# Optimization experiments

Measured on AMD Instinct MI355X. Metric: run time of the kernel, lower is better.

Reference implementation:

```python
import jax, jax.numpy as jnp
import numpy as np

N, NPER, B, E = 65536, 1024, 64, 1048576
IN_F, HID, K, NCLS = 128, 64, 16, 10


def setup_inputs() -> dict:
    key = jax.random.key(0)
    ks = jax.random.split(key, 12)
    x = jax.random.normal(ks[0], (N, IN_F), jnp.float32)
    # block-structured intra-graph edges: 64 graphs of 1024 contiguous nodes
    gid = jax.random.randint(ks[1], (E,), 0, B)
    src = gid * NPER + jax.random.randint(ks[2], (E,), 0, NPER)
    dst = gid * NPER + jax.random.randint(ks[3], (E,), 0, NPER)
    edge_index = jnp.stack([src, dst]).astype(jnp.int32)
    batch = (jnp.arange(N, dtype=jnp.int32) // NPER).astype(jnp.int32)
    def lin(k, fo, fi):
        kw, kb = jax.random.split(k)
        s = 1.0 / np.sqrt(fi)
        return (jax.random.uniform(kw, (fo, fi), jnp.float32, -s, s),
                jax.random.uniform(kb, (fo,), jnp.float32, -s, s))
    W1, b1 = lin(ks[4], HID, IN_F)
    W2, b2 = lin(ks[5], HID, HID)
    Wp, bp = lin(ks[6], K, HID)      # DMoN cluster-assignment MLP (single Linear)
    Wl, bl = lin(ks[7], NCLS, HID)   # final classifier
    return {"x": x, "edge_index": edge_index, "batch": batch,
            "W1": W1, "b1": b1, "W2": W2, "b2": b2,
            "Wp": Wp, "bp": bp, "Wl": Wl, "bl": bl}


def gcn_conv(x, src, dst, W, b):
    # GCNConv with add_self_loops=True, symmetric normalization
    n = x.shape[0]
    deg = jax.ops.segment_sum(jnp.ones(src.shape[0], x.dtype), dst,
                              num_segments=n) + 1.0  # +1 for self-loop
    dinv = jax.lax.rsqrt(deg)
    h = x @ W.T
    coef = (dinv[src] * dinv[dst])[:, None]
    agg = jax.ops.segment_sum(h[src] * coef, dst, num_segments=n)
    agg = agg + h * (dinv * dinv)[:, None]  # self-loop contribution
    return agg + b


def reference(x, edge_index, batch, W1, b1, W2, b2, Wp, bp, Wl, bl):
    src, dst = edge_index[0], edge_index[1]
    h = jax.nn.relu(gcn_conv(x, src, dst, W1, b1))
    h = jax.nn.relu(gcn_conv(h, src, dst, W2, b2))
    # to_dense_batch: graphs are equal-sized and contiguous -> reshape, mask all True
    Xb = h.reshape(B, NPER, HID)
    # DMoN cluster assignment (dropout=0.0, mask all ones)
    s = jax.nn.softmax(Xb @ Wp.T + bp, axis=-1)          # [B, NPER, K]
    Xp = jax.nn.selu(jnp.einsum('bnk,bnh->bkh', s, Xb))   # pooled clusters [B, K, HID]
    out = Xp.mean(axis=1)                                  # [B, HID]
    logits = out @ Wl.T + bl                               # [B, NCLS]
    return logits
```

## Files before the change

### kernel.cpp

```cpp
#include <hip/hip_runtime.h>
#include <cstddef>

#define N_NODES 65536
#define NPER    1024
#define NGRAPH  64
#define HID     64
#define IN_F    128
#define KCLUS   16
#define NCLS    10
#define ECAP    20480
#define HSTRIDE 12
#define ZROW    NPER
#define LIN_BLOCKS 512

template <int K>
__device__ __forceinline__ void gemm_tile(const float* __restrict__ X,
                                          const float* __restrict__ W,
                                          float* __restrict__ Y,
                                          float (*xs)[68], float (*ws)[68],
                                          int block, int t) {
    const size_t row0 = (size_t)block * 128;
    const int rbase = t >> 3;
    const int cbase = t & 7;
    float acc[4][8] = {};

    for (int kc = 0; kc < K; kc += 64) {
        __syncthreads();
        for (int i = t; i < 128 * 16; i += 256) {
            int row = i >> 4, k4 = (i & 15) << 2;
            *(float4*)&xs[row][k4] = *(const float4*)(X + (row0 + row) * K + kc + k4);
        }
        for (int i = t; i < 64 * 16; i += 256) {
            int col = i >> 4, k4 = (i & 15) << 2;
            *(float4*)&ws[col][k4] = *(const float4*)(W + col * K + kc + k4);
        }
        __syncthreads();

#pragma unroll 4
        for (int k4 = 0; k4 < 64; k4 += 4) {
            float4 xr[4], wr[8];
#pragma unroll
            for (int rr = 0; rr < 4; ++rr) xr[rr] = *(const float4*)&xs[rbase + 32 * rr][k4];
#pragma unroll
            for (int cc = 0; cc < 8; ++cc) wr[cc] = *(const float4*)&ws[cbase + 8 * cc][k4];
#pragma unroll
            for (int rr = 0; rr < 4; ++rr)
#pragma unroll
                for (int cc = 0; cc < 8; ++cc) {
                    acc[rr][cc] = fmaf(xr[rr].x, wr[cc].x, acc[rr][cc]);
                    acc[rr][cc] = fmaf(xr[rr].y, wr[cc].y, acc[rr][cc]);
                    acc[rr][cc] = fmaf(xr[rr].z, wr[cc].z, acc[rr][cc]);
                    acc[rr][cc] = fmaf(xr[rr].w, wr[cc].w, acc[rr][cc]);
                }
        }
    }

#pragma unroll
    for (int rr = 0; rr < 4; ++rr)
#pragma unroll
        for (int cc = 0; cc < 8; ++cc)
            Y[(row0 + rbase + 32 * rr) * HID + cbase + 8 * cc] = acc[rr][cc];
}

__global__ __launch_bounds__(256) void front_kernel(const float* __restrict__ X,
                                                    const float* __restrict__ W,
                                                    float* __restrict__ Y,
                                                    const int* __restrict__ src,
                                                    const int* __restrict__ dst,
                                                    int* __restrict__ ecnt,
                                                    int* __restrict__ gedges, int E) {
    __shared__ float xs[128][68];
    __shared__ float ws[64][68];
    const int t = threadIdx.x;

    if (blockIdx.x >= LIN_BLOCKS) {
        int* hist = (int*)&xs[0][0];
        int* base_l = hist + NGRAPH;
        const int e0 = (blockIdx.x - LIN_BLOCKS) * 1024;
        if (t < NGRAPH) hist[t] = 0;
        __syncthreads();

        int gg[4], rr[4], pk[4];
#pragma unroll
        for (int i = 0; i < 4; ++i) {
            int idx = e0 + i * 256 + t;
            if (idx < E) {
                int d = dst[idx], s = src[idx];
                int g = d >> 10;
                gg[i] = g;
                pk[i] = ((d & 1023) << 10) | (s & 1023);
                rr[i] = atomicAdd(&hist[g], 1);
            } else gg[i] = -1;
        }
        __syncthreads();
        if (t < NGRAPH) base_l[t] = atomicAdd(&ecnt[t], hist[t]);
        __syncthreads();
#pragma unroll
        for (int i = 0; i < 4; ++i) {
            if (gg[i] >= 0) {
                int pos = base_l[gg[i]] + rr[i];
                if (pos < ECAP) gedges[gg[i] * ECAP + pos] = pk[i];
            }
        }
        return;
    }

    gemm_tile<IN_F>(X, W, Y, xs, ws, blockIdx.x, t);
}

template <int K>
__global__ __launch_bounds__(256) void linear_kernel(const float* __restrict__ X,
                                                     const float* __restrict__ W,
                                                     float* __restrict__ Y) {
    __shared__ float xs[128][68];
    __shared__ float ws[64][68];
    gemm_tile<K>(X, W, Y, xs, ws, blockIdx.x, threadIdx.x);
}

__global__ __launch_bounds__(1024) void csr_kernel(const int* __restrict__ gedges,
                                                   const int* __restrict__ ecnt,
                                                   int* __restrict__ rp,
                                                   unsigned short* __restrict__ esorted,
                                                   float* __restrict__ dinv) {
    __shared__ int hist[NPER];
    __shared__ int wsum[16];
    const int g = blockIdx.x, t = threadIdx.x;
    const int lane = t & 63, wid = t >> 6;
    const int ec = ecnt[g];
    const int* ge = gedges + (size_t)g * ECAP;

    hist[t] = 0;
    __syncthreads();
    for (int i = t; i < ec; i += 1024) atomicAdd(&hist[ge[i] >> 10], 1);
    __syncthreads();

    const int h0 = hist[t];
    const int pd = (h0 + 3) & ~3;
    int v = pd;
#pragma unroll
    for (int off = 1; off < 64; off <<= 1) {
        int x = __shfl_up(v, off, 64);
        if (lane >= off) v += x;
    }
    if (lane == 63) wsum[wid] = v;
    __syncthreads();
    if (wid == 0) {
        int wv = (lane < 16) ? wsum[lane] : 0;
#pragma unroll
        for (int off = 1; off < 16; off <<= 1) {
            int x = __shfl_up(wv, off, 64);
            if (lane >= off) wv += x;
        }
        if (lane < 16) wsum[lane] = wv;
    }
    __syncthreads();
    const int incl = v + (wid > 0 ? wsum[wid - 1] : 0);
    const int excl = incl - pd;

    rp[g * (NPER + 1) + t] = excl;
    if (t == NPER - 1) rp[g * (NPER + 1) + NPER] = incl;
    dinv[g * NPER + t] = rsqrtf((float)h0 + 1.0f);

    hist[t] = excl;
    __syncthreads();

    unsigned short* es = esorted + (size_t)g * ECAP;
    for (int i = t; i < ec; i += 1024) {
        int pk = ge[i];
        int pos = atomicAdd(&hist[pk >> 10], 1);
        es[pos] = (unsigned short)(pk & 1023);
    }
    __syncthreads();
    for (int q = excl + h0; q < excl + pd; ++q) es[q] = (unsigned short)ZROW;
}

__global__ __launch_bounds__(512) void agg_kernel(const float* __restrict__ h,
                                                  const unsigned short* __restrict__ esorted,
                                                  const int* __restrict__ rp,
                                                  const float* __restrict__ dinv,
                                                  const float* __restrict__ bias,
                                                  float* __restrict__ outp) {
    __shared__ float Hs[(NPER + 1) * HSTRIDE];
    __shared__ float dl[NPER];
    const int g = blockIdx.x & 63;
    const int f0 = (blockIdx.x >> 6) * 8;
    const int t = threadIdx.x;
    const int base = g * NPER;

    for (int r = t; r < NPER; r += 512) {
        const float* hp = h + (size_t)(base + r) * HID + f0;
        float4 a = *(const float4*)hp;
        float4 b = *(const float4*)(hp + 4);
        float dv = dinv[base + r];
        dl[r] = dv;
        float* row = &Hs[r * HSTRIDE];
        *(float4*)row = make_float4(a.x * dv, a.y * dv, a.z * dv, a.w * dv);
        *(float4*)(row + 4) = make_float4(b.x * dv, b.y * dv, b.z * dv, b.w * dv);
    }
    if (t < HSTRIDE) Hs[ZROW * HSTRIDE + t] = 0.f;
    float bb[8];
#pragma unroll
    for (int j = 0; j < 8; ++j) bb[j] = bias[f0 + j];
    const unsigned short* es = esorted + (size_t)g * ECAP;
    const int* rpg = rp + g * (NPER + 1);
    __syncthreads();

    for (int ld = t; ld < NPER; ld += 512) {
        int p = rpg[ld];
        const int pe = rpg[ld + 1];
        const float* srow = &Hs[ld * HSTRIDE];
        float4 acc0 = *(const float4*)srow;
        float4 acc1 = *(const float4*)(srow + 4);
        float4 bcc0 = make_float4(0.f, 0.f, 0.f, 0.f);
        float4 bcc1 = make_float4(0.f, 0.f, 0.f, 0.f);

        for (; p < pe; p += 4) {
            uint2 w4 = *(const uint2*)(es + p);
            const float* r0 = &Hs[(int)(w4.x & 0xFFFFu) * HSTRIDE];
            const float* r1 = &Hs[(int)(w4.x >> 16) * HSTRIDE];
            const float* r2 = &Hs[(int)(w4.y & 0xFFFFu) * HSTRIDE];
            const float* r3 = &Hs[(int)(w4.y >> 16) * HSTRIDE];
            float4 a0 = *(const float4*)r0, a1 = *(const float4*)(r0 + 4);
            float4 b0 = *(const float4*)r1, b1 = *(const float4*)(r1 + 4);
            float4 c0v = *(const float4*)r2, c1v = *(const float4*)(r2 + 4);
            float4 d0 = *(const float4*)r3, d1 = *(const float4*)(r3 + 4);
            acc0.x += a0.x; acc0.y += a0.y; acc0.z += a0.z; acc0.w += a0.w;
            acc1.x += a1.x; acc1.y += a1.y; acc1.z += a1.z; acc1.w += a1.w;
            bcc0.x += b0.x; bcc0.y += b0.y; bcc0.z += b0.z; bcc0.w += b0.w;
            bcc1.x += b1.x; bcc1.y += b1.y; bcc1.z += b1.z; bcc1.w += b1.w;
            acc0.x += c0v.x; acc0.y += c0v.y; acc0.z += c0v.z; acc0.w += c0v.w;
            acc1.x += c1v.x; acc1.y += c1v.y; acc1.z += c1v.z; acc1.w += c1v.w;
            bcc0.x += d0.x; bcc0.y += d0.y; bcc0.z += d0.z; bcc0.w += d0.w;
            bcc1.x += d1.x; bcc1.y += d1.y; bcc1.z += d1.z; bcc1.w += d1.w;
        }
        acc0.x += bcc0.x; acc0.y += bcc0.y; acc0.z += bcc0.z; acc0.w += bcc0.w;
        acc1.x += bcc1.x; acc1.y += bcc1.y; acc1.z += bcc1.z; acc1.w += bcc1.w;

        const float dv = dl[ld];
        float4 o0, o1;
        o0.x = fmaxf(fmaf(acc0.x, dv, bb[0]), 0.f);
        o0.y = fmaxf(fmaf(acc0.y, dv, bb[1]), 0.f);
        o0.z = fmaxf(fmaf(acc0.z, dv, bb[2]), 0.f);
        o0.w = fmaxf(fmaf(acc0.w, dv, bb[3]), 0.f);
        o1.x = fmaxf(fmaf(acc1.x, dv, bb[4]), 0.f);
        o1.y = fmaxf(fmaf(acc1.y, dv, bb[5]), 0.f);
        o1.z = fmaxf(fmaf(acc1.z, dv, bb[6]), 0.f);
        o1.w = fmaxf(fmaf(acc1.w, dv, bb[7]), 0.f);
        float* op = outp + (size_t)(base + ld) * HID + f0;
        *(float4*)op = o0;
        *(float4*)(op + 4) = o1;
    }
}

__global__ __launch_bounds__(256) void pool1_kernel(const float* __restrict__ h,
                                                    const float* __restrict__ Wp,
                                                    const float* __restrict__ bp,
                                                    float* __restrict__ xpart) {
    __shared__ float xs[128][HID + 1];
    __shared__ float ss[128][KCLUS + 1];
    __shared__ float wp[KCLUS][HID];
    __shared__ float bps[KCLUS];
    const int g = blockIdx.x >> 3;
    const int c = blockIdx.x & 7;
    const int t = threadIdx.x;
    const float* hb = h + ((size_t)g * NPER + c * 128) * HID;

    for (int i = t; i < 128 * HID / 4; i += 256) {
        float4 v = ((const float4*)hb)[i];
        int row = i >> 4, col = (i & 15) * 4;
        xs[row][col] = v.x; xs[row][col + 1] = v.y; xs[row][col + 2] = v.z; xs[row][col + 3] = v.w;
    }
    for (int i = t; i < KCLUS * HID; i += 256) wp[i >> 6][i & 63] = Wp[i];
    if (t < KCLUS) bps[t] = bp[t];
    __syncthreads();

    if (t < 128) {
        float lg[KCLUS];
        float mx = -1e30f;
#pragma unroll
        for (int k = 0; k < KCLUS; ++k) {
            float a = bps[k];
#pragma unroll 8
            for (int hh = 0; hh < HID; ++hh) a = fmaf(xs[t][hh], wp[k][hh], a);
            lg[k] = a;
            mx = fmaxf(mx, a);
        }
        float sum = 0.f;
#pragma unroll
        for (int k = 0; k < KCLUS; ++k) {
            lg[k] = __expf(lg[k] - mx);
            sum += lg[k];
        }
        float inv = 1.0f / sum;
#pragma unroll
        for (int k = 0; k < KCLUS; ++k) ss[t][k] = lg[k] * inv;
    }
    __syncthreads();

    const int hcol = t & 63;
    const int k0 = (t >> 6) * 4;
    float a0 = 0.f, a1 = 0.f, a2 = 0.f, a3 = 0.f;
#pragma unroll 8
    for (int n = 0; n < 128; ++n) {
        float xv = xs[n][hcol];
        a0 = fmaf(ss[n][k0 + 0], xv, a0);
        a1 = fmaf(ss[n][k0 + 1], xv, a1);
        a2 = fmaf(ss[n][k0 + 2], xv, a2);
        a3 = fmaf(ss[n][k0 + 3], xv, a3);
    }
    float* xp = xpart + (((size_t)(g * 8 + c)) * KCLUS + k0) * HID + hcol;
    xp[0] = a0; xp[HID] = a1; xp[2 * HID] = a2; xp[3 * HID] = a3;
}

__global__ __launch_bounds__(256) void pool2_kernel(const float* __restrict__ xpart,
                                                    const float* __restrict__ Wl,
                                                    const float* __restrict__ bl,
                                                    float* __restrict__ out) {
    __shared__ float xp[KCLUS][HID + 1];
    __shared__ float outm[HID];
    const int g = blockIdx.x;
    const int t = threadIdx.x;
    const int hcol = t & 63;
    const int k0 = (t >> 6) * 4;
    const float* base = xpart + (size_t)g * 8 * KCLUS * HID;

    float a[4] = {};
#pragma unroll
    for (int c = 0; c < 8; ++c)
#pragma unroll
        for (int j = 0; j < 4; ++j)
            a[j] += base[(c * KCLUS + k0 + j) * HID + hcol];

    const float sc = 1.0507009873554805f, al = 1.6732632423543772f;
#pragma unroll
    for (int j = 0; j < 4; ++j) {
        float v = a[j];
        xp[k0 + j][hcol] = v > 0.f ? sc * v : sc * al * (__expf(v) - 1.f);
    }
    __syncthreads();

    if (t < HID) {
        float m = 0.f;
#pragma unroll
        for (int k = 0; k < KCLUS; ++k) m += xp[k][t];
        outm[t] = m * (1.0f / KCLUS);
    }
    __syncthreads();

    if (t < NCLS) {
        float acc = bl[t];
#pragma unroll 8
        for (int hh = 0; hh < HID; ++hh) acc = fmaf(outm[hh], Wl[t * HID + hh], acc);
        out[g * NCLS + t] = acc;
    }
}

extern "C" void kernel_launch(void* const* d_in, const int* in_sizes, int n_in,
                              void* d_out, int out_size, void* d_ws, size_t ws_size,
                              hipStream_t stream) {
    const float* x  = (const float*)d_in[0];
    const int* eidx = (const int*)d_in[1];
    const float* W1 = (const float*)d_in[3];
    const float* b1 = (const float*)d_in[4];
    const float* W2 = (const float*)d_in[5];
    const float* b2 = (const float*)d_in[6];
    const float* Wp = (const float*)d_in[7];
    const float* bp = (const float*)d_in[8];
    const float* Wl = (const float*)d_in[9];
    const float* bl = (const float*)d_in[10];
    float* out = (float*)d_out;

    const int E = in_sizes[1] / 2;
    const int* src = eidx;
    const int* dst = eidx + E;

    char* w = (char*)d_ws;
    int*            ecnt    = (int*)w;            w += 256;
    int*            gedges  = (int*)w;            w += (size_t)NGRAPH * ECAP * 4;
    unsigned short* esorted = (unsigned short*)w; w += (size_t)NGRAPH * ECAP * 2;
    int*            rp      = (int*)w;            w += (size_t)NGRAPH * (NPER + 1) * 4;
    float*          dinv    = (float*)w;          w += (size_t)N_NODES * 4;
    float*          A       = (float*)w;          w += (size_t)N_NODES * HID * 4;
    float*          Bf      = (float*)w;          w += (size_t)N_NODES * HID * 4;
    float*          xpart   = (float*)w;          w += (size_t)NGRAPH * 8 * KCLUS * HID * 4;

    hipMemsetAsync(ecnt, 0, 256, stream);

    const int nbucket = (E + 1023) / 1024;
    front_kernel<<<LIN_BLOCKS + nbucket, 256, 0, stream>>>(x, W1, A, src, dst, ecnt, gedges, E);
    csr_kernel<<<NGRAPH, 1024, 0, stream>>>(gedges, ecnt, rp, esorted, dinv);

    agg_kernel<<<NGRAPH * 8, 512, 0, stream>>>(A, esorted, rp, dinv, b1, Bf);

    linear_kernel<HID><<<N_NODES / 128, 256, 0, stream>>>(Bf, W2, A);
    agg_kernel<<<NGRAPH * 8, 512, 0, stream>>>(A, esorted, rp, dinv, b2, Bf);

    pool1_kernel<<<NGRAPH * 8, 256, 0, stream>>>(Bf, Wp, bp, xpart);
    pool2_kernel<<<NGRAPH, 256, 0, stream>>>(xpart, Wl, bl, out);
}
```

Measured before the change: 217.5 us.

## Fuse whole GCN pipeline into one cooperative persistent kernel with grid syncs

Replaces the seven separate kernel launches plus memset with a single cooperative mega-kernel of 512 blocks of 512 threads. Phases are separated by grid.sync(). The kernel zeroes counters in-kernel and changes CSR building to a deg/cursor atomic scatter. The intent is to remove per-launch gaps and host overhead between stages. The cost is that every phase is now tied to a fixed 512-block grid with larger blocks, and there are nine grid-wide barriers. It falls back to the old path if cooperative launch is not possible.

After: 213.9 us. Within noise of the previous version (-1.7%).

```diff
diff --git a/kernel.cpp b/kernel.cpp
--- a/kernel.cpp
+++ b/kernel.cpp
@@ -1,5 +1,8 @@
 #include <hip/hip_runtime.h>
+#include <hip/hip_cooperative_groups.h>
 #include <cstddef>
+
+namespace cg = cooperative_groups;
 
 #define N_NODES 65536
 #define NPER    1024
@@ -12,6 +15,8 @@
 #define HSTRIDE 12
 #define ZROW    NPER
 #define LIN_BLOCKS 512
+#define MGRID   512
+#define MBLK    512
 
 template <int K>
 __device__ __forceinline__ void gemm_tile(const float* __restrict__ X,
@@ -355,6 +360,346 @@
     }
 }
 
+
+struct SmGemm  { float xs[128][68]; float ws[64][68]; };
+struct SmAgg   { float Hs[(NPER + 1) * HSTRIDE]; float dl[NPER]; };
+struct SmBkt   { int hist[NGRAPH]; int base[NGRAPH]; };
+struct SmScan  { int wsum[8]; };
+struct SmPool1 { float xs[128][HID + 1]; float ss[128][KCLUS + 1];
+                 float wp[KCLUS][HID]; float bps[KCLUS]; };
+struct SmPool2 { float xp[KCLUS][HID + 1]; float outm[HID]; };
+union  SmAll   { SmGemm g; SmAgg a; SmBkt b; SmScan s; SmPool1 p1; SmPool2 p2; };
+
+struct MegaArgs {
+    const float* x; const int* src; const int* dst;
+    const float* W1; const float* b1; const float* W2; const float* b2;
+    const float* Wp; const float* bp; const float* Wl; const float* bl;
+    int* ecnt; int* gedges; int* deg; int* cursor; int* rp;
+    unsigned short* esorted; float* dinv; float* A; float* Bf; float* xpart;
+    float* out; int E;
+};
+
+template <int K>
+__device__ __forceinline__ void gemm512(const float* __restrict__ X,
+                                        const float* __restrict__ W,
+                                        float* __restrict__ Y,
+                                        float (*xs)[68], float (*ws)[68],
+                                        int block, int t) {
+    const size_t row0 = (size_t)block * 128;
+    const int rbase = t >> 3;
+    const int cbase = t & 7;
+    float acc[2][8] = {};
+
+    for (int kc = 0; kc < K; kc += 64) {
+        __syncthreads();
+        for (int i = t; i < 128 * 16; i += MBLK) {
+            int row = i >> 4, k4 = (i & 15) << 2;
+            *(float4*)&xs[row][k4] = *(const float4*)(X + (row0 + row) * K + kc + k4);
+        }
+        for (int i = t; i < 64 * 16; i += MBLK) {
+            int col = i >> 4, k4 = (i & 15) << 2;
+            *(float4*)&ws[col][k4] = *(const float4*)(W + col * K + kc + k4);
+        }
+        __syncthreads();
+
+#pragma unroll 4
+        for (int k4 = 0; k4 < 64; k4 += 4) {
+            float4 xr[2], wr[8];
+#pragma unroll
+            for (int rr = 0; rr < 2; ++rr) xr[rr] = *(const float4*)&xs[rbase + 64 * rr][k4];
+#pragma unroll
+            for (int cc = 0; cc < 8; ++cc) wr[cc] = *(const float4*)&ws[cbase + 8 * cc][k4];
+#pragma unroll
+            for (int rr = 0; rr < 2; ++rr)
+#pragma unroll
+                for (int cc = 0; cc < 8; ++cc) {
+                    acc[rr][cc] = fmaf(xr[rr].x, wr[cc].x, acc[rr][cc]);
+                    acc[rr][cc] = fmaf(xr[rr].y, wr[cc].y, acc[rr][cc]);
+                    acc[rr][cc] = fmaf(xr[rr].z, wr[cc].z, acc[rr][cc]);
+                    acc[rr][cc] = fmaf(xr[rr].w, wr[cc].w, acc[rr][cc]);
+                }
+        }
+    }
+
+#pragma unroll
+    for (int rr = 0; rr < 2; ++rr)
+#pragma unroll
+        for (int cc = 0; cc < 8; ++cc)
+            Y[(row0 + rbase + 64 * rr) * HID + cbase + 8 * cc] = acc[rr][cc];
+}
+
+__device__ __forceinline__ void agg_phase(const float* __restrict__ h,
+                                          const unsigned short* __restrict__ esorted,
+                                          const int* __restrict__ rp,
+                                          const float* __restrict__ dinv,
+                                          const float* __restrict__ bias,
+                                          float* __restrict__ outp,
+                                          SmAgg& s, int bid, int t) {
+    const int g = bid & 63;
+    const int f0 = (bid >> 6) * 8;
+    const int base = g * NPER;
+
+    for (int r = t; r < NPER; r += MBLK) {
+        const float* hp = h + (size_t)(base + r) * HID + f0;
+        float4 a = *(const float4*)hp;
+        float4 b = *(const float4*)(hp + 4);
+        float dv = dinv[base + r];
+        s.dl[r] = dv;
+        float* row = &s.Hs[r * HSTRIDE];
+        *(float4*)row = make_float4(a.x * dv, a.y * dv, a.z * dv, a.w * dv);
+        *(float4*)(row + 4) = make_float4(b.x * dv, b.y * dv, b.z * dv, b.w * dv);
+    }
+    if (t < HSTRIDE) s.Hs[ZROW * HSTRIDE + t] = 0.f;
+    float bb[8];
+#pragma unroll
+    for (int j = 0; j < 8; ++j) bb[j] = bias[f0 + j];
+    const unsigned short* es = esorted + (size_t)g * ECAP;
+    const int* rpg = rp + g * (NPER + 1);
+    __syncthreads();
+
+    for (int ld = t; ld < NPER; ld += MBLK) {
+        int p = rpg[ld];
+        const int pe = rpg[ld + 1];
+        const float* srow = &s.Hs[ld * HSTRIDE];
+        float4 acc0 = *(const float4*)srow;
+        float4 acc1 = *(const float4*)(srow + 4);
+        float4 bcc0 = make_float4(0.f, 0.f, 0.f, 0.f);
+        float4 bcc1 = make_float4(0.f, 0.f, 0.f, 0.f);
+
+        for (; p < pe; p += 4) {
+            uint2 w4 = *(const uint2*)(es + p);
+            const float* r0 = &s.Hs[(int)(w4.x & 0xFFFFu) * HSTRIDE];
+            const float* r1 = &s.Hs[(int)(w4.x >> 16) * HSTRIDE];
+            const float* r2 = &s.Hs[(int)(w4.y & 0xFFFFu) * HSTRIDE];
+            const float* r3 = &s.Hs[(int)(w4.y >> 16) * HSTRIDE];
+            float4 a0 = *(const float4*)r0, a1 = *(const float4*)(r0 + 4);
+            float4 b0 = *(const float4*)r1, b1 = *(const float4*)(r1 + 4);
+            float4 c0v = *(const float4*)r2, c1v = *(const float4*)(r2 + 4);
+            float4 d0 = *(const float4*)r3, d1 = *(const float4*)(r3 + 4);
+            acc0.x += a0.x; acc0.y += a0.y; acc0.z += a0.z; acc0.w += a0.w;
+            acc1.x += a1.x; acc1.y += a1.y; acc1.z += a1.z; acc1.w += a1.w;
+            bcc0.x += b0.x; bcc0.y += b0.y; bcc0.z += b0.z; bcc0.w += b0.w;
+            bcc1.x += b1.x; bcc1.y += b1.y; bcc1.z += b1.z; bcc1.w += b1.w;
+            acc0.x += c0v.x; acc0.y += c0v.y; acc0.z += c0v.z; acc0.w += c0v.w;
+            acc1.x += c1v.x; acc1.y += c1v.y; acc1.z += c1v.z; acc1.w += c1v.w;
+            bcc0.x += d0.x; bcc0.y += d0.y; bcc0.z += d0.z; bcc0.w += d0.w;
+            bcc1.x += d1.x; bcc1.y += d1.y; bcc1.z += d1.z; bcc1.w += d1.w;
+        }
+        acc0.x += bcc0.x; acc0.y += bcc0.y; acc0.z += bcc0.z; acc0.w += bcc0.w;
+        acc1.x += bcc1.x; acc1.y += bcc1.y; acc1.z += bcc1.z; acc1.w += bcc1.w;
+
+        const float dv = s.dl[ld];
+        float4 o0, o1;
+        o0.x = fmaxf(fmaf(acc0.x, dv, bb[0]), 0.f);
+        o0.y = fmaxf(fmaf(acc0.y, dv, bb[1]), 0.f);
+        o0.z = fmaxf(fmaf(acc0.z, dv, bb[2]), 0.f);
+        o0.w = fmaxf(fmaf(acc0.w, dv, bb[3]), 0.f);
+        o1.x = fmaxf(fmaf(acc1.x, dv, bb[4]), 0.f);
+        o1.y = fmaxf(fmaf(acc1.y, dv, bb[5]), 0.f);
+        o1.z = fmaxf(fmaf(acc1.z, dv, bb[6]), 0.f);
+        o1.w = fmaxf(fmaf(acc1.w, dv, bb[7]), 0.f);
+        float* op = outp + (size_t)(base + ld) * HID + f0;
+        *(float4*)op = o0;
+        *(float4*)(op + 4) = o1;
+    }
+}
+
+__global__ __launch_bounds__(MBLK, 4) void mega_kernel(MegaArgs a) {
+    cg::grid_group grid = cg::this_grid();
+    __shared__ SmAll sm;
+    const int bid = blockIdx.x;
+    const int t = threadIdx.x;
+
+    {
+        int gid = bid * MBLK + t;
+        if (gid < NGRAPH) a.ecnt[gid] = 0;
+        if (gid < N_NODES) a.deg[gid] = 0;
+    }
+    grid.sync();
+
+    {
+        int* hist = sm.b.hist;
+        int* basel = sm.b.base;
+        if (t < NGRAPH) hist[t] = 0;
+        __syncthreads();
+        int gg[4], rr2[4], pk[4];
+        const int e0 = bid * 2048;
+#pragma unroll
+        for (int i = 0; i < 4; ++i) {
+            int idx = e0 + i * MBLK + t;
+            if (idx < a.E) {
+                int d = a.dst[idx], s = a.src[idx];
+                int g = d >> 10;
+                gg[i] = g;
+                pk[i] = ((d & 1023) << 10) | (s & 1023);
+                rr2[i] = atomicAdd(&hist[g], 1);
+                atomicAdd(&a.deg[d], 1);
+            } else gg[i] = -1;
+        }
+        __syncthreads();
+        if (t < NGRAPH) basel[t] = atomicAdd(&a.ecnt[t], hist[t]);
+        __syncthreads();
+#pragma unroll
+        for (int i = 0; i < 4; ++i)
+            if (gg[i] >= 0) {
+                int pos = basel[gg[i]] + rr2[i];
+                if (pos < ECAP) a.gedges[gg[i] * ECAP + pos] = pk[i];
+            }
+    }
+    gemm512<IN_F>(a.x, a.W1, a.A, sm.g.xs, sm.g.ws, bid, t);
+    grid.sync();
+
+    if (bid < NGRAPH) {
+        const int g = bid;
+        int2 dd = *(const int2*)(a.deg + g * NPER + 2 * t);
+        const int d0 = dd.x, d1 = dd.y;
+        const int pd0 = (d0 + 3) & ~3, pd1 = (d1 + 3) & ~3;
+        const int v = pd0 + pd1;
+        const int lane = t & 63, w = t >> 6;
+        int vs = v;
+#pragma unroll
+        for (int off = 1; off < 64; off <<= 1) {
+            int xv = __shfl_up(vs, off, 64);
+            if (lane >= off) vs += xv;
+        }
+        if (lane == 63) sm.s.wsum[w] = vs;
+        __syncthreads();
+        if (t < 8) {
+            int wv = sm.s.wsum[t];
+#pragma unroll
+            for (int off = 1; off < 8; off <<= 1) {
+                int xv = __shfl_up(wv, off, 8);
+                if (t >= off) wv += xv;
+            }
+            sm.s.wsum[t] = wv;
+        }
+        __syncthreads();
+        const int incl = vs + (w > 0 ? sm.s.wsum[w - 1] : 0);
+        const int excl = incl - v;
+        const int e1 = excl + pd0;
+        int* rpg = a.rp + g * (NPER + 1);
+        rpg[2 * t] = excl;
+        rpg[2 * t + 1] = e1;
+        if (t == MBLK - 1) rpg[NPER] = incl;
+        a.cursor[g * NPER + 2 * t] = excl;
+        a.cursor[g * NPER + 2 * t + 1] = e1;
+        a.dinv[g * NPER + 2 * t] = rsqrtf((float)d0 + 1.0f);
+        a.dinv[g * NPER + 2 * t + 1] = rsqrtf((float)d1 + 1.0f);
+    }
+    grid.sync();
+
+    {
+        const int g = bid >> 3;
+        const int vt = ((bid & 7) << 9) | t;
+        const int ec = a.ecnt[g];
+        const int* ge = a.gedges + (size_t)g * ECAP;
+        unsigned short* es = a.esorted + (size_t)g * ECAP;
+        for (int i = vt; i < ec; i += 4096) {
+            int pkv = ge[i];
+            int pos = atomicAdd(&a.cursor[g * NPER + (pkv >> 10)], 1);
+            if (pos < ECAP) es[pos] = (unsigned short)(pkv & 1023);
+        }
+        if (vt < NPER) {
+            const int excl = a.rp[g * (NPER + 1) + vt];
+            const int h0 = a.deg[g * NPER + vt];
+            const int pd = (h0 + 3) & ~3;
+            for (int q = excl + h0; q < excl + pd; ++q) es[q] = (unsigned short)ZROW;
+        }
+    }
+    grid.sync();
+
+    agg_phase(a.A, a.esorted, a.rp, a.dinv, a.b1, a.Bf, sm.a, bid, t);
+    grid.sync();
+
+    gemm512<HID>(a.Bf, a.W2, a.A, sm.g.xs, sm.g.ws, bid, t);
+    grid.sync();
+
+    agg_phase(a.A, a.esorted, a.rp, a.dinv, a.b2, a.Bf, sm.a, bid, t);
+    grid.sync();
+
+    {
+        const int g = bid >> 3;
+        const int c = bid & 7;
+        const float* hb = a.Bf + ((size_t)g * NPER + c * 128) * HID;
+        for (int i = t; i < 128 * HID / 4; i += MBLK) {
+            float4 v = ((const float4*)hb)[i];
+            int row = i >> 4, col = (i & 15) * 4;
+            sm.p1.xs[row][col] = v.x; sm.p1.xs[row][col + 1] = v.y;
+            sm.p1.xs[row][col + 2] = v.z; sm.p1.xs[row][col + 3] = v.w;
+        }
+        for (int i = t; i < KCLUS * HID; i += MBLK) sm.p1.wp[i >> 6][i & 63] = a.Wp[i];
+        if (t < KCLUS) sm.p1.bps[t] = a.bp[t];
+        __syncthreads();
+
+        if (t < 128) {
+            float lg[KCLUS];
+            float mx = -1e30f;
+#pragma unroll
+            for (int k = 0; k < KCLUS; ++k) {
+                float acc = sm.p1.bps[k];
+#pragma unroll 8
+                for (int hh = 0; hh < HID; ++hh) acc = fmaf(sm.p1.xs[t][hh], sm.p1.wp[k][hh], acc);
+                lg[k] = acc;
+                mx = fmaxf(mx, acc);
+            }
+            float sum = 0.f;
+#pragma unroll
+            for (int k = 0; k < KCLUS; ++k) {
+                lg[k] = __expf(lg[k] - mx);
+                sum += lg[k];
+            }
+            float inv = 1.0f / sum;
+#pragma unroll
+            for (int k = 0; k < KCLUS; ++k) sm.p1.ss[t][k] = lg[k] * inv;
+        }
+        __syncthreads();
+
+        const int hcol = t & 63;
+        const int k0 = (t >> 6) * 2;
+        float a0 = 0.f, a1 = 0.f;
+#pragma unroll 8
+        for (int n = 0; n < 128; ++n) {
+            float xv = sm.p1.xs[n][hcol];
+            a0 = fmaf(sm.p1.ss[n][k0], xv, a0);
+            a1 = fmaf(sm.p1.ss[n][k0 + 1], xv, a1);
+        }
+        float* xp = a.xpart + (((size_t)(g * 8 + c)) * KCLUS + k0) * HID + hcol;
+        xp[0] = a0;
+        xp[HID] = a1;
+    }
+    grid.sync();
+
+    if (bid < NGRAPH) {
+        const int g = bid;
+        const int hcol = t & 63;
+        const int k0 = (t >> 6) * 2;
+        const float* basep = a.xpart + (size_t)g * 8 * KCLUS * HID;
+        float v0 = 0.f, v1 = 0.f;
+#pragma unroll
+        for (int c = 0; c < 8; ++c) {
+            v0 += basep[(c * KCLUS + k0) * HID + hcol];
+            v1 += basep[(c * KCLUS + k0 + 1) * HID + hcol];
+        }
+        const float sc = 1.0507009873554805f, al = 1.6732632423543772f;
+        sm.p2.xp[k0][hcol]     = v0 > 0.f ? sc * v0 : sc * al * (__expf(v0) - 1.f);
+        sm.p2.xp[k0 + 1][hcol] = v1 > 0.f ? sc * v1 : sc * al * (__expf(v1) - 1.f);
+        __syncthreads();
+        if (t < HID) {
+            float m = 0.f;
+#pragma unroll
+            for (int k = 0; k < KCLUS; ++k) m += sm.p2.xp[k][t];
+            sm.p2.outm[t] = m * (1.0f / KCLUS);
+        }
+        __syncthreads();
+        if (t < NCLS) {
+            float acc = a.bl[t];
+#pragma unroll 8
+            for (int hh = 0; hh < HID; ++hh) acc = fmaf(sm.p2.outm[hh], a.Wl[t * HID + hh], acc);
+            a.out[g * NCLS + t] = acc;
+        }
+    }
+}
+
 extern "C" void kernel_launch(void* const* d_in, const int* in_sizes, int n_in,
                               void* d_out, int out_size, void* d_ws, size_t ws_size,
                               hipStream_t stream) {
@@ -383,6 +728,40 @@
     float*          A       = (float*)w;          w += (size_t)N_NODES * HID * 4;
     float*          Bf      = (float*)w;          w += (size_t)N_NODES * HID * 4;
     float*          xpart   = (float*)w;          w += (size_t)NGRAPH * 8 * KCLUS * HID * 4;
+    int*            deg     = (int*)w;            w += (size_t)N_NODES * 4;
+    int*            cursor  = (int*)w;            w += (size_t)N_NODES * 4;
+
+    static int coop_cached = -1;
+    if (coop_cached < 0) {
+        coop_cached = 0;
+        int dev = 0;
+        if (hipGetDevice(&dev) == hipSuccess) {
+            hipDeviceProp_t prop;
+            int nb = 0;
+            if (hipGetDeviceProperties(&prop, dev) == hipSuccess &&
+                prop.cooperativeLaunch &&
+                hipOccupancyMaxActiveBlocksPerMultiprocessor(
+                    &nb, (const void*)mega_kernel, MBLK, 0) == hipSuccess &&
+                nb >= 2 && nb * prop.multiProcessorCount >= MGRID)
+                coop_cached = 1;
+        }
+    }
+
+    if (coop_cached == 1 && E <= MGRID * 2048) {
+        MegaArgs ha;
+        ha.x = x; ha.src = src; ha.dst = dst;
+        ha.W1 = W1; ha.b1 = b1; ha.W2 = W2; ha.b2 = b2;
+        ha.Wp = Wp; ha.bp = bp; ha.Wl = Wl; ha.bl = bl;
+        ha.ecnt = ecnt; ha.gedges = gedges; ha.deg = deg; ha.cursor = cursor; ha.rp = rp;
+        ha.esorted = esorted; ha.dinv = dinv; ha.A = A; ha.Bf = Bf; ha.xpart = xpart;
+        ha.out = out; ha.E = E;
+        void* args[] = { &ha };
+        if (hipLaunchCooperativeKernel((const void*)mega_kernel, dim3(MGRID), dim3(MBLK),
+                                       args, 0, stream) == hipSuccess)
+            return;
+        (void)hipGetLastError();
+        coop_cached = 0;
+    }
 
     hipMemsetAsync(ecnt, 0, 256, stream);
 
```

## Split CSR build across 8 blocks per graph and fuse pooling via last-block reduction

Applied to the files above, without the earlier changes.

Degree counting moves into the front bucketing pass as global atomics, so the CSR step no longer needs a per-graph histogram pass. The scatter is then spread over 8 blocks per graph (512 blocks instead of 64), each redundantly computing the prefix scan and using global atomic cursors. The two pooling kernels are fused with a threadfence and done-counter so the last block of each graph does the final reduction and classifier. The cost is many more global atomics on deg and czero, plus a larger memset to clear them.

New measurement: 328.6 us. 1.51x slower.

```diff
diff --git a/kernel.cpp b/kernel.cpp
--- a/kernel.cpp
+++ b/kernel.cpp
@@ -68,7 +68,8 @@
                                                     const int* __restrict__ src,
                                                     const int* __restrict__ dst,
                                                     int* __restrict__ ecnt,
-                                                    int* __restrict__ gedges, int E) {
+                                                    int* __restrict__ gedges,
+                                                    int* __restrict__ deg, int E) {
     __shared__ float xs[128][68];
     __shared__ float ws[64][68];
     const int t = threadIdx.x;
@@ -90,6 +91,7 @@
                 gg[i] = g;
                 pk[i] = ((d & 1023) << 10) | (s & 1023);
                 rr[i] = atomicAdd(&hist[g], 1);
+                atomicAdd(&deg[d], 1);
             } else gg[i] = -1;
         }
         __syncthreads();
@@ -117,61 +119,72 @@
     gemm_tile<K>(X, W, Y, xs, ws, blockIdx.x, threadIdx.x);
 }
 
-__global__ __launch_bounds__(1024) void csr_kernel(const int* __restrict__ gedges,
-                                                   const int* __restrict__ ecnt,
-                                                   int* __restrict__ rp,
-                                                   unsigned short* __restrict__ esorted,
-                                                   float* __restrict__ dinv) {
-    __shared__ int hist[NPER];
-    __shared__ int wsum[16];
-    const int g = blockIdx.x, t = threadIdx.x;
-    const int lane = t & 63, wid = t >> 6;
+__global__ __launch_bounds__(512) void scatter_kernel(const int* __restrict__ gedges,
+                                                      const int* __restrict__ ecnt,
+                                                      const int* __restrict__ deg,
+                                                      int* __restrict__ czero,
+                                                      int* __restrict__ rp,
+                                                      unsigned short* __restrict__ esorted,
+                                                      float* __restrict__ dinv) {
+    __shared__ int rps[NPER];
+    __shared__ int wsum[8];
+    const int g = blockIdx.x >> 3;
+    const int sub = blockIdx.x & 7;
+    const int t = threadIdx.x;
+    const int lane = t & 63, w = t >> 6;
+
+    int2 dd = *(const int2*)(deg + g * NPER + 2 * t);
+    const int d0 = dd.x, d1 = dd.y;
+    const int pd0 = (d0 + 3) & ~3, pd1 = (d1 + 3) & ~3;
+    const int v = pd0 + pd1;
+    int vs = v;
+#pragma unroll
+    for (int off = 1; off < 64; off <<= 1) {
+        int xv = __shfl_up(vs, off, 64);
+        if (lane >= off) vs += xv;
+    }
+    if (lane == 63) wsum[w] = vs;
+    __syncthreads();
+    if (t < 8) {
+        int wv = wsum[t];
+#pragma unroll
+        for (int off = 1; off < 8; off <<= 1) {
+            int xv = __shfl_up(wv, off, 8);
+            if (t >= off) wv += xv;
+        }
+        wsum[t] = wv;
+    }
+    __syncthreads();
+    const int incl = vs + (w > 0 ? wsum[w - 1] : 0);
+    const int excl = incl - v;
+    const int e1 = excl + pd0;
+    rps[2 * t] = excl;
+    rps[2 * t + 1] = e1;
+
+    if (sub == 0) {
+        int* rpg = rp + g * (NPER + 1);
+        rpg[2 * t] = excl;
+        rpg[2 * t + 1] = e1;
+        if (t == 511) rpg[NPER] = incl;
+        dinv[g * NPER + 2 * t] = rsqrtf((float)d0 + 1.0f);
+        dinv[g * NPER + 2 * t + 1] = rsqrtf((float)d1 + 1.0f);
+    }
+    __syncthreads();
+
     const int ec = ecnt[g];
     const int* ge = gedges + (size_t)g * ECAP;
-
-    hist[t] = 0;
-    __syncthreads();
-    for (int i = t; i < ec; i += 1024) atomicAdd(&hist[ge[i] >> 10], 1);
-    __syncthreads();
-
-    const int h0 = hist[t];
-    const int pd = (h0 + 3) & ~3;
-    int v = pd;
-#pragma unroll
-    for (int off = 1; off < 64; off <<= 1) {
-        int x = __shfl_up(v, off, 64);
-        if (lane >= off) v += x;
-    }
-    if (lane == 63) wsum[wid] = v;
-    __syncthreads();
-    if (wid == 0) {
-        int wv = (lane < 16) ? wsum[lane] : 0;
-#pragma unroll
-        for (int off = 1; off < 16; off <<= 1) {
-            int x = __shfl_up(wv, off, 64);
-            if (lane >= off) wv += x;
-        }
-        if (lane < 16) wsum[lane] = wv;
-    }
-    __syncthreads();
-    const int incl = v + (wid > 0 ? wsum[wid - 1] : 0);
-    const int excl = incl - pd;
-
-    rp[g * (NPER + 1) + t] = excl;
-    if (t == NPER - 1) rp[g * (NPER + 1) + NPER] = incl;
-    dinv[g * NPER + t] = rsqrtf((float)h0 + 1.0f);
-
-    hist[t] = excl;
-    __syncthreads();
-
     unsigned short* es = esorted + (size_t)g * ECAP;
-    for (int i = t; i < ec; i += 1024) {
-        int pk = ge[i];
-        int pos = atomicAdd(&hist[pk >> 10], 1);
-        es[pos] = (unsigned short)(pk & 1023);
-    }
-    __syncthreads();
-    for (int q = excl + h0; q < excl + pd; ++q) es[q] = (unsigned short)ZROW;
+    for (int i = (sub << 9) | t; i < ec; i += 4096) {
+        int pkv = ge[i];
+        int d = pkv >> 10;
+        int pos = rps[d] + atomicAdd(&czero[g * NPER + d], 1);
+        if (pos < ECAP) es[pos] = (unsigned short)(pkv & 1023);
+    }
+
+    if (sub == 1) {
+        for (int q = excl + d0; q < excl + pd0; ++q) es[q] = (unsigned short)ZROW;
+        for (int q = e1 + d1; q < e1 + pd1; ++q) es[q] = (unsigned short)ZROW;
+    }
 }
 
 __global__ __launch_bounds__(512) void agg_kernel(const float* __restrict__ h,
@@ -252,14 +265,21 @@
     }
 }
 
-__global__ __launch_bounds__(256) void pool1_kernel(const float* __restrict__ h,
-                                                    const float* __restrict__ Wp,
-                                                    const float* __restrict__ bp,
-                                                    float* __restrict__ xpart) {
+__global__ __launch_bounds__(256) void pool_kernel(const float* __restrict__ h,
+                                                   const float* __restrict__ Wp,
+                                                   const float* __restrict__ bp,
+                                                   const float* __restrict__ Wl,
+                                                   const float* __restrict__ bl,
+                                                   float* __restrict__ xpart,
+                                                   int* __restrict__ done,
+                                                   float* __restrict__ out) {
     __shared__ float xs[128][HID + 1];
     __shared__ float ss[128][KCLUS + 1];
     __shared__ float wp[KCLUS][HID];
     __shared__ float bps[KCLUS];
+    __shared__ float xp2[KCLUS][HID + 1];
+    __shared__ float outm[HID];
+    __shared__ int lastf;
     const int g = blockIdx.x >> 3;
     const int c = blockIdx.x & 7;
     const int t = threadIdx.x;
@@ -310,39 +330,33 @@
     }
     float* xp = xpart + (((size_t)(g * 8 + c)) * KCLUS + k0) * HID + hcol;
     xp[0] = a0; xp[HID] = a1; xp[2 * HID] = a2; xp[3 * HID] = a3;
-}
-
-__global__ __launch_bounds__(256) void pool2_kernel(const float* __restrict__ xpart,
-                                                    const float* __restrict__ Wl,
-                                                    const float* __restrict__ bl,
-                                                    float* __restrict__ out) {
-    __shared__ float xp[KCLUS][HID + 1];
-    __shared__ float outm[HID];
-    const int g = blockIdx.x;
-    const int t = threadIdx.x;
-    const int hcol = t & 63;
-    const int k0 = (t >> 6) * 4;
-    const float* base = xpart + (size_t)g * 8 * KCLUS * HID;
-
+
+    __threadfence();
+    if (t == 0) lastf = (atomicAdd(&done[g], 1) == 7) ? 1 : 0;
+    __syncthreads();
+    if (!lastf) return;
+    __threadfence();
+
+    const float* basep = xpart + (size_t)g * 8 * KCLUS * HID;
     float a[4] = {};
 #pragma unroll
-    for (int c = 0; c < 8; ++c)
+    for (int cc = 0; cc < 8; ++cc)
 #pragma unroll
         for (int j = 0; j < 4; ++j)
-            a[j] += base[(c * KCLUS + k0 + j) * HID + hcol];
+            a[j] += basep[(cc * KCLUS + k0 + j) * HID + hcol];
 
     const float sc = 1.0507009873554805f, al = 1.6732632423543772f;
 #pragma unroll
     for (int j = 0; j < 4; ++j) {
         float v = a[j];
-        xp[k0 + j][hcol] = v > 0.f ? sc * v : sc * al * (__expf(v) - 1.f);
+        xp2[k0 + j][hcol] = v > 0.f ? sc * v : sc * al * (__expf(v) - 1.f);
     }
     __syncthreads();
 
     if (t < HID) {
         float m = 0.f;
 #pragma unroll
-        for (int k = 0; k < KCLUS; ++k) m += xp[k][t];
+        for (int k = 0; k < KCLUS; ++k) m += xp2[k][t];
         outm[t] = m * (1.0f / KCLUS);
     }
     __syncthreads();
@@ -376,6 +390,10 @@
 
     char* w = (char*)d_ws;
     int*            ecnt    = (int*)w;            w += 256;
+    int*            done    = (int*)w;            w += 256;
+    int*            deg     = (int*)w;            w += (size_t)N_NODES * 4;
+    int*            czero   = (int*)w;            w += (size_t)N_NODES * 4;
+    const size_t zero_bytes = (size_t)(w - (char*)d_ws);
     int*            gedges  = (int*)w;            w += (size_t)NGRAPH * ECAP * 4;
     unsigned short* esorted = (unsigned short*)w; w += (size_t)NGRAPH * ECAP * 2;
     int*            rp      = (int*)w;            w += (size_t)NGRAPH * (NPER + 1) * 4;
@@ -384,17 +402,17 @@
     float*          Bf      = (float*)w;          w += (size_t)N_NODES * HID * 4;
     float*          xpart   = (float*)w;          w += (size_t)NGRAPH * 8 * KCLUS * HID * 4;
 
-    hipMemsetAsync(ecnt, 0, 256, stream);
+    hipMemsetAsync(d_ws, 0, zero_bytes, stream);
 
     const int nbucket = (E + 1023) / 1024;
-    front_kernel<<<LIN_BLOCKS + nbucket, 256, 0, stream>>>(x, W1, A, src, dst, ecnt, gedges, E);
-    csr_kernel<<<NGRAPH, 1024, 0, stream>>>(gedges, ecnt, rp, esorted, dinv);
+    front_kernel<<<LIN_BLOCKS + nbucket, 256, 0, stream>>>(x, W1, A, src, dst, ecnt, gedges, deg, E);
+
+    scatter_kernel<<<NGRAPH * 8, 512, 0, stream>>>(gedges, ecnt, deg, czero, rp, esorted, dinv);
 
     agg_kernel<<<NGRAPH * 8, 512, 0, stream>>>(A, esorted, rp, dinv, b1, Bf);
 
     linear_kernel<HID><<<N_NODES / 128, 256, 0, stream>>>(Bf, W2, A);
     agg_kernel<<<NGRAPH * 8, 512, 0, stream>>>(A, esorted, rp, dinv, b2, Bf);
 
-    pool1_kernel<<<NGRAPH * 8, 256, 0, stream>>>(Bf, Wp, bp, xpart);
-    pool2_kernel<<<NGRAPH, 256, 0, stream>>>(xpart, Wl, bl, out);
-}
+    pool_kernel<<<NGRAPH * 8, 256, 0, stream>>>(Bf, Wp, bp, Wl, bl, xpart, done, out);
+}
```

## Replace two-pass CSR build with fixed-capacity per-node adjacency slots

Applied to the files above, without the earlier changes.

Drops the per-graph bucketing plus the separate CSR sort kernel. Edges are now scattered directly into a fixed 64-slot padded adjacency list per destination node using global atomics on a per-node degree counter, and dinv is computed on the fly inside the aggregation. This removes one kernel launch and one full pass over the edges, at the cost of global atomic contention and a memset of the degree array. Any node with more than 64 in-edges would be silently truncated; average degree is 16, so the cap is probably not hit.

After: 227.0 us. 4.3% more time.

```diff
diff --git a/kernel.cpp b/kernel.cpp
--- a/kernel.cpp
+++ b/kernel.cpp
@@ -8,9 +8,8 @@
 #define IN_F    128
 #define KCLUS   16
 #define NCLS    10
-#define ECAP    20480
+#define NCAP    64
 #define HSTRIDE 12
-#define ZROW    NPER
 #define LIN_BLOCKS 512
 
 template <int K>
@@ -67,39 +66,21 @@
                                                     float* __restrict__ Y,
                                                     const int* __restrict__ src,
                                                     const int* __restrict__ dst,
-                                                    int* __restrict__ ecnt,
-                                                    int* __restrict__ gedges, int E) {
+                                                    int* __restrict__ deg,
+                                                    unsigned short* __restrict__ es, int E) {
     __shared__ float xs[128][68];
     __shared__ float ws[64][68];
     const int t = threadIdx.x;
 
     if (blockIdx.x >= LIN_BLOCKS) {
-        int* hist = (int*)&xs[0][0];
-        int* base_l = hist + NGRAPH;
         const int e0 = (blockIdx.x - LIN_BLOCKS) * 1024;
-        if (t < NGRAPH) hist[t] = 0;
-        __syncthreads();
-
-        int gg[4], rr[4], pk[4];
 #pragma unroll
         for (int i = 0; i < 4; ++i) {
             int idx = e0 + i * 256 + t;
             if (idx < E) {
                 int d = dst[idx], s = src[idx];
-                int g = d >> 10;
-                gg[i] = g;
-                pk[i] = ((d & 1023) << 10) | (s & 1023);
-                rr[i] = atomicAdd(&hist[g], 1);
-            } else gg[i] = -1;
-        }
-        __syncthreads();
-        if (t < NGRAPH) base_l[t] = atomicAdd(&ecnt[t], hist[t]);
-        __syncthreads();
-#pragma unroll
-        for (int i = 0; i < 4; ++i) {
-            if (gg[i] >= 0) {
-                int pos = base_l[gg[i]] + rr[i];
-                if (pos < ECAP) gedges[gg[i] * ECAP + pos] = pk[i];
+                int pos = atomicAdd(&deg[d], 1);
+                if (pos < NCAP) es[(size_t)d * NCAP + pos] = (unsigned short)(s & 1023);
             }
         }
         return;
@@ -117,70 +98,12 @@
     gemm_tile<K>(X, W, Y, xs, ws, blockIdx.x, threadIdx.x);
 }
 
-__global__ __launch_bounds__(1024) void csr_kernel(const int* __restrict__ gedges,
-                                                   const int* __restrict__ ecnt,
-                                                   int* __restrict__ rp,
-                                                   unsigned short* __restrict__ esorted,
-                                                   float* __restrict__ dinv) {
-    __shared__ int hist[NPER];
-    __shared__ int wsum[16];
-    const int g = blockIdx.x, t = threadIdx.x;
-    const int lane = t & 63, wid = t >> 6;
-    const int ec = ecnt[g];
-    const int* ge = gedges + (size_t)g * ECAP;
-
-    hist[t] = 0;
-    __syncthreads();
-    for (int i = t; i < ec; i += 1024) atomicAdd(&hist[ge[i] >> 10], 1);
-    __syncthreads();
-
-    const int h0 = hist[t];
-    const int pd = (h0 + 3) & ~3;
-    int v = pd;
-#pragma unroll
-    for (int off = 1; off < 64; off <<= 1) {
-        int x = __shfl_up(v, off, 64);
-        if (lane >= off) v += x;
-    }
-    if (lane == 63) wsum[wid] = v;
-    __syncthreads();
-    if (wid == 0) {
-        int wv = (lane < 16) ? wsum[lane] : 0;
-#pragma unroll
-        for (int off = 1; off < 16; off <<= 1) {
-            int x = __shfl_up(wv, off, 64);
-            if (lane >= off) wv += x;
-        }
-        if (lane < 16) wsum[lane] = wv;
-    }
-    __syncthreads();
-    const int incl = v + (wid > 0 ? wsum[wid - 1] : 0);
-    const int excl = incl - pd;
-
-    rp[g * (NPER + 1) + t] = excl;
-    if (t == NPER - 1) rp[g * (NPER + 1) + NPER] = incl;
-    dinv[g * NPER + t] = rsqrtf((float)h0 + 1.0f);
-
-    hist[t] = excl;
-    __syncthreads();
-
-    unsigned short* es = esorted + (size_t)g * ECAP;
-    for (int i = t; i < ec; i += 1024) {
-        int pk = ge[i];
-        int pos = atomicAdd(&hist[pk >> 10], 1);
-        es[pos] = (unsigned short)(pk & 1023);
-    }
-    __syncthreads();
-    for (int q = excl + h0; q < excl + pd; ++q) es[q] = (unsigned short)ZROW;
-}
-
 __global__ __launch_bounds__(512) void agg_kernel(const float* __restrict__ h,
-                                                  const unsigned short* __restrict__ esorted,
-                                                  const int* __restrict__ rp,
-                                                  const float* __restrict__ dinv,
+                                                  const unsigned short* __restrict__ es,
+                                                  const int* __restrict__ deg,
                                                   const float* __restrict__ bias,
                                                   float* __restrict__ outp) {
-    __shared__ float Hs[(NPER + 1) * HSTRIDE];
+    __shared__ float Hs[NPER * HSTRIDE];
     __shared__ float dl[NPER];
     const int g = blockIdx.x & 63;
     const int f0 = (blockIdx.x >> 6) * 8;
@@ -191,31 +114,31 @@
         const float* hp = h + (size_t)(base + r) * HID + f0;
         float4 a = *(const float4*)hp;
         float4 b = *(const float4*)(hp + 4);
-        float dv = dinv[base + r];
+        float dv = rsqrtf((float)deg[base + r] + 1.0f);
         dl[r] = dv;
         float* row = &Hs[r * HSTRIDE];
         *(float4*)row = make_float4(a.x * dv, a.y * dv, a.z * dv, a.w * dv);
         *(float4*)(row + 4) = make_float4(b.x * dv, b.y * dv, b.z * dv, b.w * dv);
     }
-    if (t < HSTRIDE) Hs[ZROW * HSTRIDE + t] = 0.f;
     float bb[8];
 #pragma unroll
     for (int j = 0; j < 8; ++j) bb[j] = bias[f0 + j];
-    const unsigned short* es = esorted + (size_t)g * ECAP;
-    const int* rpg = rp + g * (NPER + 1);
     __syncthreads();
 
     for (int ld = t; ld < NPER; ld += 512) {
-        int p = rpg[ld];
-        const int pe = rpg[ld + 1];
+        const unsigned short* ep = es + (size_t)(base + ld) * NCAP;
+        int dg = deg[base + ld];
+        dg = dg < NCAP ? dg : NCAP;
         const float* srow = &Hs[ld * HSTRIDE];
         float4 acc0 = *(const float4*)srow;
         float4 acc1 = *(const float4*)(srow + 4);
         float4 bcc0 = make_float4(0.f, 0.f, 0.f, 0.f);
         float4 bcc1 = make_float4(0.f, 0.f, 0.f, 0.f);
 
-        for (; p < pe; p += 4) {
-            uint2 w4 = *(const uint2*)(es + p);
+        int p = 0;
+        const int p4 = dg & ~3;
+        for (; p < p4; p += 4) {
+            uint2 w4 = *(const uint2*)(ep + p);
             const float* r0 = &Hs[(int)(w4.x & 0xFFFFu) * HSTRIDE];
             const float* r1 = &Hs[(int)(w4.x >> 16) * HSTRIDE];
             const float* r2 = &Hs[(int)(w4.y & 0xFFFFu) * HSTRIDE];
@@ -233,6 +156,12 @@
             bcc0.x += d0.x; bcc0.y += d0.y; bcc0.z += d0.z; bcc0.w += d0.w;
             bcc1.x += d1.x; bcc1.y += d1.y; bcc1.z += d1.z; bcc1.w += d1.w;
         }
+        for (; p < dg; ++p) {
+            const float* rr = &Hs[(int)ep[p] * HSTRIDE];
+            float4 e0 = *(const float4*)rr, e1 = *(const float4*)(rr + 4);
+            acc0.x += e0.x; acc0.y += e0.y; acc0.z += e0.z; acc0.w += e0.w;
+            acc1.x += e1.x; acc1.y += e1.y; acc1.z += e1.z; acc1.w += e1.w;
+        }
         acc0.x += bcc0.x; acc0.y += bcc0.y; acc0.z += bcc0.z; acc0.w += bcc0.w;
         acc1.x += bcc1.x; acc1.y += bcc1.y; acc1.z += bcc1.z; acc1.w += bcc1.w;
 
@@ -375,25 +304,21 @@
     const int* dst = eidx + E;
 
     char* w = (char*)d_ws;
-    int*            ecnt    = (int*)w;            w += 256;
-    int*            gedges  = (int*)w;            w += (size_t)NGRAPH * ECAP * 4;
-    unsigned short* esorted = (unsigned short*)w; w += (size_t)NGRAPH * ECAP * 2;
-    int*            rp      = (int*)w;            w += (size_t)NGRAPH * (NPER + 1) * 4;
-    float*          dinv    = (float*)w;          w += (size_t)N_NODES * 4;
-    float*          A       = (float*)w;          w += (size_t)N_NODES * HID * 4;
-    float*          Bf      = (float*)w;          w += (size_t)N_NODES * HID * 4;
-    float*          xpart   = (float*)w;          w += (size_t)NGRAPH * 8 * KCLUS * HID * 4;
-
-    hipMemsetAsync(ecnt, 0, 256, stream);
-
-    const int nbucket = (E + 1023) / 1024;
-    front_kernel<<<LIN_BLOCKS + nbucket, 256, 0, stream>>>(x, W1, A, src, dst, ecnt, gedges, E);
-    csr_kernel<<<NGRAPH, 1024, 0, stream>>>(gedges, ecnt, rp, esorted, dinv);
-
-    agg_kernel<<<NGRAPH * 8, 512, 0, stream>>>(A, esorted, rp, dinv, b1, Bf);
+    int*            deg   = (int*)w;            w += (size_t)N_NODES * 4;
+    unsigned short* es    = (unsigned short*)w; w += (size_t)N_NODES * NCAP * 2;
+    float*          A     = (float*)w;          w += (size_t)N_NODES * HID * 4;
+    float*          Bf    = (float*)w;          w += (size_t)N_NODES * HID * 4;
+    float*          xpart = (float*)w;          w += (size_t)NGRAPH * 8 * KCLUS * HID * 4;
+
+    hipMemsetAsync(deg, 0, (size_t)N_NODES * 4, stream);
+
+    const int nbuild = (E + 1023) / 1024;
+    front_kernel<<<LIN_BLOCKS + nbuild, 256, 0, stream>>>(x, W1, A, src, dst, deg, es, E);
+
+    agg_kernel<<<NGRAPH * 8, 512, 0, stream>>>(A, es, deg, b1, Bf);
 
     linear_kernel<HID><<<N_NODES / 128, 256, 0, stream>>>(Bf, W2, A);
-    agg_kernel<<<NGRAPH * 8, 512, 0, stream>>>(A, esorted, rp, dinv, b2, Bf);
+    agg_kernel<<<NGRAPH * 8, 512, 0, stream>>>(A, es, deg, b2, Bf);
 
     pool1_kernel<<<NGRAPH * 8, 256, 0, stream>>>(Bf, Wp, bp, xpart);
     pool2_kernel<<<NGRAPH, 256, 0, stream>>>(xpart, Wl, bl, out);
```
